# Optimization experiments

Measured on AMD Instinct MI355X. Metric: run time of the kernel, lower is better.

The kernel has to match this reference:

```python
import jax, jax.numpy as jnp
import numpy as np


def _flip(x, c):
    # reflection about index c along the last (W) axis: out[..., i] = x[..., (c - i) mod W]
    W = x.shape[-1]
    idx = (c - jnp.arange(W)) % W
    return x[..., idx]


def setup_inputs() -> dict:
    key = jax.random.key(0)
    k1, k2, k3 = jax.random.split(key, 3)
    B, C, H, W = 8, 32, 256, 256
    x = jax.random.normal(k1, (B, C, H, W), dtype=jnp.float32)
    s = jax.random.normal(k2, (B, 11), dtype=jnp.float32)
    w = jax.random.uniform(k3, (B, 1, H, W), dtype=jnp.float32)
    w_param = jnp.ones((1,), dtype=jnp.float32)
    b_param = jnp.zeros((1,), dtype=jnp.float32)
    return {"x": x, "s": s, "w": w, "w_param": w_param, "b_param": b_param}


def reference(x, s, w, w_param, b_param):
    B, C, H, W = x.shape
    step = W // 8  # 32 for W=256
    # s -> sigmoid(w*s + b), shape [B, 11, 1, 1]
    sg = jax.nn.sigmoid(w_param * s + b_param).reshape(B, -1, 1, 1)
    # 7 circular shifts (45..315 deg) + 4 reflections
    a = w * x
    b = w
    for i in range(7):  # shifts step*1 .. step*7, gated by sg[:, 0..6]
        n = step * (i + 1)
        wk = sg[:, i:i + 1] * jnp.roll(w, n, axis=3)
        a = a + wk * jnp.roll(x, n, axis=3)
        b = b + wk
    for j in range(4):  # flips about step*1-1 .. step*4-1, gated by sg[:, 7..10]
        c = step * (j + 1) - 1
        wk = sg[:, 7 + j:8 + j] * _flip(w, c)
        a = a + wk * _flip(x, c)
        b = b + wk
    return a / b
```

## Files before the change

### kernel.cpp

```cpp
#include <hip/hip_runtime.h>
#include <math.h>

#define BB 8
#define CC 32
#define HH 256
#define WW 256

__device__ __forceinline__ float half_mirror(float v) {
    int i = __builtin_bit_cast(int, v);
    i = __builtin_amdgcn_update_dpp(i, i, 0x141, 0xf, 0xf, true);
    return __builtin_bit_cast(float, i);
}

__global__ __launch_bounds__(256, 2)
void symctrl2_kernel(const float* __restrict__ x,
                     const float* __restrict__ s,
                     const float* __restrict__ wg,
                     const float* __restrict__ w_param,
                     const float* __restrict__ b_param,
                     float* __restrict__ out) {
    const int bh  = blockIdx.x;
    const int b   = bh >> 8;
    const int h   = bh & (HH - 1);
    const int wv  = threadIdx.x >> 6;
    const int l   = threadIdx.x & 63;
    const int row = l >> 3;
    const int u   = l & 7;
    const int c   = (wv << 3) + row;

    const float* wrow = wg  + ((size_t)b * HH + h) * WW;
    const float* xrow = x   + (((size_t)b * CC + c) * HH + h) * WW;
    float*       orow = out + (((size_t)b * CC + c) * HH + h) * WW;

    float4 wq[8], xq[8];
    #pragma unroll
    for (int q = 0; q < 8; ++q)
        wq[q] = *reinterpret_cast<const float4*>(wrow + 32 * q + 4 * u);
    #pragma unroll
    for (int q = 0; q < 8; ++q)
        xq[q] = *reinterpret_cast<const float4*>(xrow + 32 * q + 4 * u);

    const float wp = w_param[0], bpv = b_param[0];
    float gk[8], gf[4];
    gk[0] = 1.0f;
    #pragma unroll
    for (int k = 0; k < 7; ++k) {
        float v = wp * s[b * 11 + k] + bpv;
        gk[k + 1] = 1.0f / (1.0f + __expf(-v));
    }
    #pragma unroll
    for (int j = 0; j < 4; ++j) {
        float v = wp * s[b * 11 + 7 + j] + bpv;
        gf[j] = 1.0f / (1.0f + __expf(-v));
    }

    float den[8][4];
    #pragma unroll
    for (int g = 0; g < 8; ++g) {
        float d0 = 0.f, d1 = 0.f, d2 = 0.f, d3 = 0.f;
        #pragma unroll
        for (int k = 0; k < 8; ++k) {
            const float4 w4 = wq[(g - k) & 7];
            d0 = fmaf(gk[k], w4.x, d0);
            d1 = fmaf(gk[k], w4.y, d1);
            d2 = fmaf(gk[k], w4.z, d2);
            d3 = fmaf(gk[k], w4.w, d3);
        }
        den[g][0] = d0; den[g][1] = d1; den[g][2] = d2; den[g][3] = d3;
    }
    #pragma unroll
    for (int q = 0; q < 8; ++q) {
        const float m0 = half_mirror(wq[q].x);
        const float m1 = half_mirror(wq[q].y);
        const float m2 = half_mirror(wq[q].z);
        const float m3 = half_mirror(wq[q].w);
        #pragma unroll
        for (int j = 0; j < 4; ++j) {
            const int g = (j - q) & 7;
            den[g][0] = fmaf(gf[j], m3, den[g][0]);
            den[g][1] = fmaf(gf[j], m2, den[g][1]);
            den[g][2] = fmaf(gf[j], m1, den[g][2]);
            den[g][3] = fmaf(gf[j], m0, den[g][3]);
        }
    }
    float rden[8][4];
    #pragma unroll
    for (int g = 0; g < 8; ++g)
        #pragma unroll
        for (int e = 0; e < 4; ++e)
            rden[g][e] = __builtin_amdgcn_rcpf(den[g][e]);

    float P[8][4];
    #pragma unroll
    for (int q = 0; q < 8; ++q) {
        P[q][0] = wq[q].x * xq[q].x;
        P[q][1] = wq[q].y * xq[q].y;
        P[q][2] = wq[q].z * xq[q].z;
        P[q][3] = wq[q].w * xq[q].w;
    }
    float num[8][4];
    #pragma unroll
    for (int g = 0; g < 8; ++g) {
        float n0 = 0.f, n1 = 0.f, n2 = 0.f, n3 = 0.f;
        #pragma unroll
        for (int k = 0; k < 8; ++k) {
            const int q = (g - k) & 7;
            n0 = fmaf(gk[k], P[q][0], n0);
            n1 = fmaf(gk[k], P[q][1], n1);
            n2 = fmaf(gk[k], P[q][2], n2);
            n3 = fmaf(gk[k], P[q][3], n3);
        }
        num[g][0] = n0; num[g][1] = n1; num[g][2] = n2; num[g][3] = n3;
    }
    #pragma unroll
    for (int q = 0; q < 8; ++q) {
        const float m0 = half_mirror(P[q][0]);
        const float m1 = half_mirror(P[q][1]);
        const float m2 = half_mirror(P[q][2]);
        const float m3 = half_mirror(P[q][3]);
        #pragma unroll
        for (int j = 0; j < 4; ++j) {
            const int g = (j - q) & 7;
            num[g][0] = fmaf(gf[j], m3, num[g][0]);
            num[g][1] = fmaf(gf[j], m2, num[g][1]);
            num[g][2] = fmaf(gf[j], m1, num[g][2]);
            num[g][3] = fmaf(gf[j], m0, num[g][3]);
        }
    }
    #pragma unroll
    for (int g = 0; g < 8; ++g) {
        float4 o;
        o.x = num[g][0] * rden[g][0];
        o.y = num[g][1] * rden[g][1];
        o.z = num[g][2] * rden[g][2];
        o.w = num[g][3] * rden[g][3];
        *reinterpret_cast<float4*>(orow + 32 * g + 4 * u) = o;
    }
}

extern "C" void kernel_launch(void* const* d_in, const int* in_sizes, int n_in,
                              void* d_out, int out_size, void* d_ws, size_t ws_size,
                              hipStream_t stream) {
    const float* x  = (const float*)d_in[0];
    const float* s  = (const float*)d_in[1];
    const float* w  = (const float*)d_in[2];
    const float* wp = (const float*)d_in[3];
    const float* bp = (const float*)d_in[4];
    float* outp = (float*)d_out;

    dim3 grid(BB * HH);
    dim3 block(256);
    symctrl2_kernel<<<grid, block, 0, stream>>>(x, s, w, wp, bp, outp);
}
```

Baseline: 120.0 us.

## Precompute reciprocal denominator per row in separate kernel, raise occupancy of main

Splits the denominator computation, which depends only on w and the gates and not on the channel, into a small pre-kernel that writes reciprocal denominators per (b,h) row to workspace. The main kernel then loads them instead of recomputing them redundantly for every channel, which lowers register pressure and allows the launch bound to rise to 4 blocks per CU. The cost is an extra kernel launch plus an extra workspace write and read of B*H*W floats, and a dependence on the workspace size.

```diff
diff --git a/kernel.cpp b/kernel.cpp
--- a/kernel.cpp
+++ b/kernel.cpp
@@ -6,31 +6,61 @@
 #define HH 256
 #define WW 256
 
+__global__ __launch_bounds__(256)
+void den_kernel(const float* __restrict__ s,
+                const float* __restrict__ wg,
+                const float* __restrict__ w_param,
+                const float* __restrict__ b_param,
+                float* __restrict__ rden_out) {
+    const int bh = blockIdx.x;
+    const int b  = bh >> 8;
+    const int i  = threadIdx.x;
+
+    const float* wrow = wg + (size_t)bh * WW;
+    const float wp = w_param[0], bpv = b_param[0];
+    float g[11];
+    #pragma unroll
+    for (int k = 0; k < 11; ++k)
+        g[k] = 1.0f / (1.0f + __expf(-(wp * s[b * 11 + k] + bpv)));
+
+    float den = wrow[i];
+    #pragma unroll
+    for (int k = 1; k <= 7; ++k)
+        den = fmaf(g[k - 1], wrow[(i - 32 * k) & (WW - 1)], den);
+    #pragma unroll
+    for (int j = 0; j < 4; ++j)
+        den = fmaf(g[7 + j], wrow[(32 * j + 31 - i) & (WW - 1)], den);
+
+    rden_out[(size_t)bh * WW + i] = __builtin_amdgcn_rcpf(den);
+}
+
 __device__ __forceinline__ float half_mirror(float v) {
     int i = __builtin_bit_cast(int, v);
     i = __builtin_amdgcn_update_dpp(i, i, 0x141, 0xf, 0xf, true);
     return __builtin_bit_cast(float, i);
 }
 
-__global__ __launch_bounds__(256, 2)
-void symctrl2_kernel(const float* __restrict__ x,
-                     const float* __restrict__ s,
-                     const float* __restrict__ wg,
-                     const float* __restrict__ w_param,
-                     const float* __restrict__ b_param,
-                     float* __restrict__ out) {
+__global__ __launch_bounds__(256, 4)
+void symctrl2_main(const float* __restrict__ x,
+                   const float* __restrict__ s,
+                   const float* __restrict__ wg,
+                   const float* __restrict__ w_param,
+                   const float* __restrict__ b_param,
+                   const float* __restrict__ rden,
+                   float* __restrict__ out) {
     const int bh  = blockIdx.x;
     const int b   = bh >> 8;
-    const int h   = bh & (HH - 1);
     const int wv  = threadIdx.x >> 6;
     const int l   = threadIdx.x & 63;
     const int row = l >> 3;
     const int u   = l & 7;
     const int c   = (wv << 3) + row;
 
-    const float* wrow = wg  + ((size_t)b * HH + h) * WW;
-    const float* xrow = x   + (((size_t)b * CC + c) * HH + h) * WW;
-    float*       orow = out + (((size_t)b * CC + c) * HH + h) * WW;
+    const float* wrow = wg   + (size_t)bh * WW;
+    const float* rrow = rden + (size_t)bh * WW;
+    const size_t xoff = (((size_t)b * CC + c) * HH + (bh & (HH - 1))) * WW;
+    const float* xrow = x + xoff;
+    float*       orow = out + xoff;
 
     float4 wq[8], xq[8];
     #pragma unroll
@@ -44,51 +74,11 @@
     float gk[8], gf[4];
     gk[0] = 1.0f;
     #pragma unroll
-    for (int k = 0; k < 7; ++k) {
-        float v = wp * s[b * 11 + k] + bpv;
-        gk[k + 1] = 1.0f / (1.0f + __expf(-v));
-    }
+    for (int k = 0; k < 7; ++k)
+        gk[k + 1] = 1.0f / (1.0f + __expf(-(wp * s[b * 11 + k] + bpv)));
     #pragma unroll
-    for (int j = 0; j < 4; ++j) {
-        float v = wp * s[b * 11 + 7 + j] + bpv;
-        gf[j] = 1.0f / (1.0f + __expf(-v));
-    }
-
-    float den[8][4];
-    #pragma unroll
-    for (int g = 0; g < 8; ++g) {
-        float d0 = 0.f, d1 = 0.f, d2 = 0.f, d3 = 0.f;
-        #pragma unroll
-        for (int k = 0; k < 8; ++k) {
-            const float4 w4 = wq[(g - k) & 7];
-            d0 = fmaf(gk[k], w4.x, d0);
-            d1 = fmaf(gk[k], w4.y, d1);
-            d2 = fmaf(gk[k], w4.z, d2);
-            d3 = fmaf(gk[k], w4.w, d3);
-        }
-        den[g][0] = d0; den[g][1] = d1; den[g][2] = d2; den[g][3] = d3;
-    }
-    #pragma unroll
-    for (int q = 0; q < 8; ++q) {
-        const float m0 = half_mirror(wq[q].x);
-        const float m1 = half_mirror(wq[q].y);
-        const float m2 = half_mirror(wq[q].z);
-        const float m3 = half_mirror(wq[q].w);
-        #pragma unroll
-        for (int j = 0; j < 4; ++j) {
-            const int g = (j - q) & 7;
-            den[g][0] = fmaf(gf[j], m3, den[g][0]);
-            den[g][1] = fmaf(gf[j], m2, den[g][1]);
-            den[g][2] = fmaf(gf[j], m1, den[g][2]);
-            den[g][3] = fmaf(gf[j], m0, den[g][3]);
-        }
-    }
-    float rden[8][4];
-    #pragma unroll
-    for (int g = 0; g < 8; ++g)
-        #pragma unroll
-        for (int e = 0; e < 4; ++e)
-            rden[g][e] = __builtin_amdgcn_rcpf(den[g][e]);
+    for (int j = 0; j < 4; ++j)
+        gf[j] = 1.0f / (1.0f + __expf(-(wp * s[b * 11 + 7 + j] + bpv)));
 
     float P[8][4];
     #pragma unroll
@@ -98,6 +88,13 @@
         P[q][2] = wq[q].z * xq[q].z;
         P[q][3] = wq[q].w * xq[q].w;
     }
+    asm volatile("" ::: "memory");
+
+    float4 rq[8];
+    #pragma unroll
+    for (int g = 0; g < 8; ++g)
+        rq[g] = *reinterpret_cast<const float4*>(rrow + 32 * g + 4 * u);
+
     float num[8][4];
     #pragma unroll
     for (int g = 0; g < 8; ++g) {
@@ -130,10 +127,10 @@
     #pragma unroll
     for (int g = 0; g < 8; ++g) {
         float4 o;
-        o.x = num[g][0] * rden[g][0];
-        o.y = num[g][1] * rden[g][1];
-        o.z = num[g][2] * rden[g][2];
-        o.w = num[g][3] * rden[g][3];
+        o.x = num[g][0] * rq[g].x;
+        o.y = num[g][1] * rq[g].y;
+        o.z = num[g][2] * rq[g].z;
+        o.w = num[g][3] * rq[g].w;
         *reinterpret_cast<float4*>(orow + 32 * g + 4 * u) = o;
     }
 }
@@ -147,8 +144,9 @@
     const float* wp = (const float*)d_in[3];
     const float* bp = (const float*)d_in[4];
     float* outp = (float*)d_out;
+    float* rden = (float*)d_ws;
 
     dim3 grid(BB * HH);
-    dim3 block(256);
-    symctrl2_kernel<<<grid, block, 0, stream>>>(x, s, w, wp, bp, outp);
+    den_kernel<<<grid, dim3(WW), 0, stream>>>(s, w, wp, bp, rden);
+    symctrl2_main<<<grid, dim3(256), 0, stream>>>(x, s, w, wp, bp, rden, outp);
 }
```

New measurement: 123.9 us. 3.3% more time.
